# Kernel optimization log

Hardware: AMD Instinct MI355X
Metric: run time of the kernel (lower is better)

## Reference

```python
import jax, jax.numpy as jnp
import numpy as np

EPS = 1e-5
B, H, W = 128, 98, 40

def _conv2d(x, w):
    return jax.lax.conv_general_dilated(x, w, (1, 1), 'VALID', dimension_numbers=('NCHW', 'OIHW', 'NCHW'))

def _bn_ch(x, g, b):
    # BatchNorm over (B,H,W) per channel (training-mode batch stats, as in the torch default mode)
    m = jnp.mean(x, (0, 2, 3), keepdims=True)
    v = jnp.var(x, (0, 2, 3), keepdims=True)
    return (x - m) * jax.lax.rsqrt(v + EPS) * g[None, :, None, None] + b[None, :, None, None]

def _bn_all(x, g, b):
    # BatchNorm3d(1): single channel -> normalize over the whole tensor
    m = jnp.mean(x)
    v = jnp.var(x)
    return (x - m) * jax.lax.rsqrt(v + EPS) * g[0] + b[0]

def _lc(h, w, b):
    # 62 distinct tiny Conv3d(1,1,(3,1,1)) == locally-connected window-3 conv over channel axis: 64 -> 62
    out = b[None, :, None, None]
    for k in range(3):
        out = out + h[:, k:k + 62] * w[None, :, k, None, None]
    return out

def _lc_block(h, lcw, lcb, gs, bs, Wm, bm, gm, bbm):
    h = jax.nn.relu(_bn_all(_lc(h, lcw, lcb), gs, bs))
    # Conv3d kernel (62,1,1): pure channel mixing 62 -> 64 (no relu after, matching torch code)
    h = jnp.einsum('bdhw,cd->bchw', h, Wm) + bm[None, :, None, None]
    return _bn_ch(h, gm, bbm)

def setup_inputs():
    ks = iter(jax.random.split(jax.random.key(0), 64))
    def rn(shape, s=0.05):
        return jax.random.normal(next(ks), shape, jnp.float32) * s
    d = {}
    d['x'] = jax.random.normal(next(ks), (B, H * 0 + 98 if False else 1, 98, 40), jnp.float32) if False else jax.random.normal(next(ks), (B, 1, H, W), jnp.float32)
    d['W11'] = rn((64, 1, 20, 8)); d['b11'] = rn((64,)); d['g11'] = jnp.ones((64,), jnp.float32); d['be11'] = jnp.zeros((64,), jnp.float32)
    d['lc1_w'] = rn((62, 3), 0.3); d['lc1_b'] = rn((62,)); d['g12'] = jnp.ones((1,), jnp.float32); d['be12'] = jnp.zeros((1,), jnp.float32)
    d['W13'] = rn((64, 62)); d['b13'] = rn((64,)); d['g13'] = jnp.ones((64,), jnp.float32); d['be13'] = jnp.zeros((64,), jnp.float32)
    d['W21'] = rn((64, 64, 15, 8), 0.01); d['b21'] = rn((64,)); d['g21'] = jnp.ones((64,), jnp.float32); d['be21'] = jnp.zeros((64,), jnp.float32)
    d['lc2_w'] = rn((62, 3), 0.3); d['lc2_b'] = rn((62,)); d['g22'] = jnp.ones((1,), jnp.float32); d['be22'] = jnp.zeros((1,), jnp.float32)
    d['W23'] = rn((64, 62)); d['b23'] = rn((64,)); d['g23'] = jnp.ones((64,), jnp.float32); d['be23'] = jnp.zeros((64,), jnp.float32)
    d['W31'] = rn((64, 64, 10, 8), 0.01); d['b31'] = rn((64,)); d['g31'] = jnp.ones((64,), jnp.float32); d['be31'] = jnp.zeros((64,), jnp.float32)
    d['lc3_w'] = rn((62, 3), 0.3); d['lc3_b'] = rn((62,)); d['g32'] = jnp.ones((1,), jnp.float32); d['be32'] = jnp.zeros((1,), jnp.float32)
    d['W33'] = rn((64, 62)); d['b33'] = rn((64,)); d['g33'] = jnp.ones((64,), jnp.float32); d['be33'] = jnp.zeros((64,), jnp.float32)
    d['Wf1'] = rn((64, 64 * 56 * 19), 0.01); d['bf1'] = rn((64,)); d['gf'] = jnp.ones((64,), jnp.float32); d['bef'] = jnp.zeros((64,), jnp.float32)
    d['Wf2'] = rn((35, 64)); d['bf2'] = rn((35,))
    return d

def reference(x, W11, b11, g11, be11, lc1_w, lc1_b, g12, be12, W13, b13, g13, be13, W21, b21, g21, be21, lc2_w, lc2_b, g22, be22, W23, b23, g23, be23, W31, b31, g31, be31, lc3_w, lc3_b, g32, be32, W33, b33, g33, be33, Wf1, bf1, gf, bef, Wf2, bf2):
    h = jax.nn.relu(_bn_ch(_conv2d(x, W11) + b11[None, :, None, None], g11, be11))      # [B,64,79,33]
    h = _lc_block(h, lc1_w, lc1_b, g12, be12, W13, b13, g13, be13)                       # [B,64,79,33]
    h = jax.nn.relu(_bn_ch(_conv2d(h, W21) + b21[None, :, None, None], g21, be21))       # [B,64,65,26]
    h = _lc_block(h, lc2_w, lc2_b, g22, be22, W23, b23, g23, be23)                       # [B,64,65,26]
    h = jax.nn.relu(_bn_ch(_conv2d(h, W31) + b31[None, :, None, None], g31, be31))       # [B,64,56,19]
    h = _lc_block(h, lc3_w, lc3_b, g32, be32, W33, b33, g33, be33)                       # [B,64,56,19]
    h = h.reshape(h.shape[0], -1)                                                        # [B,68096]
    h = h @ Wf1.T + bf1
    m = jnp.mean(h, 0)
    v = jnp.var(h, 0)
    h = jax.nn.relu((h - m) * jax.lax.rsqrt(v + EPS) * gf + bef)
    return h @ Wf2.T + bf2
```

## Files before the change

kernel.cpp:

```cpp
#include <hip/hip_runtime.h>

typedef __bf16 bfrag __attribute__((ext_vector_type(8)));
typedef float ffrag __attribute__((ext_vector_type(16)));

constexpr int Bn  = 128;
constexpr int H0  = 98, Wi0 = 40;
constexpr int KH1 = 20, KW1 = 8, H1 = 79, Wo1 = 33, P1 = H1 * Wo1;
constexpr int KH2 = 15, KW2 = 8, H2 = 65, Wo2 = 26, P2 = H2 * Wo2;
constexpr int KH3 = 10, KW3 = 8, H3 = 56, Wo3 = 19, P3 = H3 * Wo3;
constexpr int M1  = Bn * P1;
constexpr int M2  = Bn * P2;
constexpr int M3  = Bn * P3;
constexpr int KFC = 64 * P3;
constexpr int FCCH = 112;
constexpr int FCKL = KFC / FCCH;
constexpr int FCKS = FCKL / 16;
constexpr float EPSF = 1e-5f;

constexpr size_t oA   = 0;
constexpr size_t oB   = oA  + (size_t)Bn * 64 * P1;
constexpr size_t oHB  = oB;
constexpr size_t oWF  = oB  + 4358144;
constexpr size_t oW2  = oB  + (size_t)Bn * 62 * P1;
constexpr size_t oW3  = oW2 + 245760;
constexpr size_t oW1  = oW3 + 163840;
constexpr size_t oWM  = oW1 + 5120;
constexpr size_t oBF  = oWM + 6144;
constexpr size_t oP   = oBF + 128;
constexpr size_t oSt  = oP  + (size_t)FCCH * 8192;
constexpr size_t oF   = oSt + 9 * 512;

__device__ __forceinline__ float wred(float v) {
    #pragma unroll
    for (int o = 32; o > 0; o >>= 1) v += __shfl_down(v, o);
    return v;
}

__device__ __forceinline__ float bank4(const float* stp, int c) {
    return stp[c] + stp[128 + c] + stp[256 + c] + stp[384 + c];
}

constexpr int NZ  = 9 * 512;
constexpr int NW1 = 10240;
constexpr int NWM = 3 * 4096;
constexpr int NPREP = NZ + NW1 + NWM;
__global__ __launch_bounds__(256) void k_prep_all(
    const float* __restrict__ W11, const float* __restrict__ W13,
    const float* __restrict__ W23, const float* __restrict__ W33,
    __bf16* __restrict__ wq1, __bf16* __restrict__ wqm,
    float* __restrict__ st)
{
    int idx = blockIdx.x * 256 + threadIdx.x;
    if (idx < NZ) { st[idx] = 0.f; return; }
    idx -= NZ;
    if (idx < NW1) {
        int j = idx & 7, oc = (idx >> 3) & 63, khh = idx >> 9;
        wq1[idx] = (__bf16)W11[(size_t)oc * 160 + khh * 8 + j];
        return;
    }
    idx -= NW1;
    if (idx < NWM) {
        int which = idx >> 12, r = idx & 4095;
        int j = r & 7, oc = (r >> 3) & 63, sub = (r >> 9) & 1, ks = r >> 10;
        int k = ks * 16 + sub * 8 + j;
        const float* Wm = which == 0 ? W13 : (which == 1 ? W23 : W33);
        wqm[idx] = (k < 62) ? (__bf16)Wm[oc * 62 + k] : (__bf16)0.f;
    }
}

template <int KH, int KW>
__global__ __launch_bounds__(256) void k_foldw(
    const float* __restrict__ W, const float* __restrict__ stp,
    const float* __restrict__ g, const float* __restrict__ be,
    float inv, const float* __restrict__ bias,
    __bf16* __restrict__ wqf, float* __restrict__ biasf)
{
    constexpr int KK = KH * KW;
    __shared__ float sSc[64], sSh[64], ls[4];
    const int t = threadIdx.x;
    if (t < 64) {
        float mm = bank4(stp, t) * inv;
        float vv = bank4(stp, 64 + t) * inv - mm * mm;
        float sc = g[t] * rsqrtf(vv + EPSF);
        sSc[t] = sc;
        sSh[t] = be[t] - mm * sc;
    }
    __syncthreads();
    const int oc = blockIdx.x;
    float local = 0.f;
    for (int i = t; i < 64 * KK; i += 256) {
        int ic = i / KK, rem = i - ic * KK;
        int kh = rem / KW, kw = rem - kh * KW;
        float wv = W[(((size_t)oc * 64 + ic) * KH + kh) * KW + kw];
        int c = ic >> 4, sub = (ic >> 3) & 1, j = ic & 7, pos = kh * KW + kw;
        wqf[(size_t)pos * 4096 + c * 1024 + sub * 512 + oc * 8 + j] = (__bf16)(wv * sSc[ic]);
        local += wv * sSh[ic];
    }
    local = wred(local);
    int wv2 = t >> 6, ln = t & 63;
    if (ln == 0) ls[wv2] = local;
    __syncthreads();
    if (t == 0) biasf[oc] = bias[oc] + ls[0] + ls[1] + ls[2] + ls[3];
}

constexpr int C1COPY = 1736;
__global__ __launch_bounds__(256, 2) void k_conv1m(
    const float* __restrict__ x, const __bf16* __restrict__ wq,
    const float* __restrict__ bias, float* __restrict__ out,
    float* __restrict__ sto)
{
    const int b = blockIdx.y;
    const int m0 = blockIdx.x * 512;
    const int t = threadIdx.x, lane = t & 63, wv = t >> 6;
    const int l31 = lane & 31, lh = lane >> 5;
    __shared__ __align__(16) __bf16 X8[8 * C1COPY];

    const int oh_lo = m0 / Wo1;
    int abase[4];
    #pragma unroll
    for (int mt = 0; mt < 4; ++mt) {
        int m = m0 + wv * 128 + mt * 32 + l31;
        int mc = m > P1 - 1 ? P1 - 1 : m;
        int oh = mc / Wo1, ow = mc - oh * Wo1;
        int s = ow & 7;
        abase[mt] = s * C1COPY + (oh - oh_lo) * 48 + (ow - s);
    }
    for (int idx = t; idx < 8 * 36 * 6; idx += 256) {
        int s = idx / 216; int rr = idx - s * 216;
        int r = rr / 6, q = rr - r * 6;
        int ih = oh_lo + r; if (ih > H0 - 1) ih = H0 - 1;
        const float* src = x + ((size_t)b * H0 + ih) * Wi0;
        __bf16 tmp[8] __attribute__((aligned(16)));
        #pragma unroll
        for (int j = 0; j < 8; ++j) {
            int col = q * 8 + s + j; if (col > Wi0 - 1) col = Wi0 - 1;
            tmp[j] = (__bf16)src[col];
        }
        *(uint4*)&X8[s * C1COPY + r * 48 + q * 8] = *(uint4*)tmp;
    }
    __syncthreads();

    ffrag acc[4][2] = {};
    #pragma unroll 1
    for (int st2 = 0; st2 < 10; ++st2) {
        const int khl = st2 * 2 + lh;
        const __bf16* wp = wq + ((size_t)khl * 64 + l31) * 8;
        bfrag b0 = *(const bfrag*)(wp);
        bfrag b1 = *(const bfrag*)(wp + 256);
        #pragma unroll
        for (int mt = 0; mt < 4; ++mt) {
            bfrag a = *(const bfrag*)&X8[abase[mt] + khl * 48];
            acc[mt][0] = __builtin_amdgcn_mfma_f32_32x32x16_bf16(a, b0, acc[mt][0], 0, 0, 0);
            acc[mt][1] = __builtin_amdgcn_mfma_f32_32x32x16_bf16(a, b1, acc[mt][1], 0, 0, 0);
        }
    }

    float sS[2] = {0.f, 0.f}, sSS[2] = {0.f, 0.f};
    #pragma unroll
    for (int nt = 0; nt < 2; ++nt) {
        int oc = nt * 32 + l31;
        float bv = bias[oc];
        float* op = out + ((size_t)b * 64 + oc) * P1;
        #pragma unroll
        for (int mt = 0; mt < 4; ++mt) {
            int mbase = m0 + wv * 128 + mt * 32 + lh * 4;
            #pragma unroll
            for (int g = 0; g < 4; ++g) {
                int mr = mbase + g * 8;
                float v0 = acc[mt][nt][g * 4 + 0] + bv;
                float v1 = acc[mt][nt][g * 4 + 1] + bv;
                float v2 = acc[mt][nt][g * 4 + 2] + bv;
                float v3 = acc[mt][nt][g * 4 + 3] + bv;
                if (mr + 1 < P1) {
                    *(float2*)(op + mr) = make_float2(v0, v1);
                    sS[nt] += v0 + v1; sSS[nt] += v0 * v0 + v1 * v1;
                    if (mr + 3 < P1) {
                        *(float2*)(op + mr + 2) = make_float2(v2, v3);
                        sS[nt] += v2 + v3; sSS[nt] += v2 * v2 + v3 * v3;
                    } else if (mr + 2 < P1) {
                        op[mr + 2] = v2; sS[nt] += v2; sSS[nt] += v2 * v2;
                    }
                } else if (mr < P1) {
                    op[mr] = v0; sS[nt] += v0; sSS[nt] += v0 * v0;
                }
            }
        }
    }
    #pragma unroll
    for (int nt = 0; nt < 2; ++nt) {
        sS[nt]  += __shfl_down(sS[nt], 32);
        sSS[nt] += __shfl_down(sSS[nt], 32);
    }
    __syncthreads();
    float* redS  = (float*)X8;
    float* redSS = redS + 256;
    if (lane < 32) {
        #pragma unroll
        for (int nt = 0; nt < 2; ++nt) {
            redS[wv * 64 + nt * 32 + l31]  = sS[nt];
            redSS[wv * 64 + nt * 32 + l31] = sSS[nt];
        }
    }
    __syncthreads();
    if (t < 64) {
        int bank = ((blockIdx.x ^ blockIdx.y) & 3) * 128;
        atomicAdd(&sto[bank + t],      redS[t] + redS[64 + t] + redS[128 + t] + redS[192 + t]);
        atomicAdd(&sto[bank + 64 + t], redSS[t] + redSS[64 + t] + redSS[128 + t] + redSS[192 + t]);
    }
}

template <int POS>
__global__ __launch_bounds__(256) void k_lc(const float* __restrict__ in,
                                            const float* __restrict__ stp,
                                            const float* __restrict__ g,
                                            const float* __restrict__ be,
                                            float inv,
                                            const float* __restrict__ lcw,
                                            const float* __restrict__ lcb,
                                            __bf16* __restrict__ Z,
                                            float* __restrict__ sto) {
    __shared__ float sAff[128];
    __shared__ float sred[4], ssred[4];
    if (threadIdx.x < 64) {
        int tt = threadIdx.x;
        float mm = bank4(stp, tt) * inv;
        float vv = bank4(stp, 64 + tt) * inv - mm * mm;
        float sc = g[tt] * rsqrtf(vv + EPSF);
        sAff[tt] = sc;
        sAff[64 + tt] = be[tt] - mm * sc;
    }
    __syncthreads();
    int morig = blockIdx.x * 256 + threadIdx.x;
    bool valid = morig < Bn * POS;
    int m = valid ? morig : Bn * POS - 1;
    int b = m / POS; int p = m - b * POS;
    const float* ip = in + (size_t)b * 64 * POS + p;
    __bf16 zb[64] __attribute__((aligned(16)));
    zb[62] = (__bf16)0.f; zb[63] = (__bf16)0.f;
    float ts = 0.f, tss = 0.f;
    float y0 = fmaxf(sAff[0] * ip[0]           + sAff[64], 0.f);
    float y1 = fmaxf(sAff[1] * ip[(size_t)POS] + sAff[65], 0.f);
    for (int c = 0; c < 62; ++c) {
        float y2 = fmaxf(sAff[c + 2] * ip[(size_t)(c + 2) * POS] + sAff[64 + c + 2], 0.f);
        float o = lcb[c] + y0 * lcw[c * 3] + y1 * lcw[c * 3 + 1] + y2 * lcw[c * 3 + 2];
        zb[c] = (__bf16)o;
        if (valid) { ts += o; tss += o * o; }
        y0 = y1; y1 = y2;
    }
    __bf16* zp = Z + (size_t)m * 64;
    #pragma unroll
    for (int j = 0; j < 8; ++j)
        *(uint4*)(zp + j * 8) = *(uint4*)(zb + j * 8);
    ts = wred(ts); tss = wred(tss);
    int wv = threadIdx.x >> 6, ln = threadIdx.x & 63;
    if (ln == 0) { sred[wv] = ts; ssred[wv] = tss; }
    __syncthreads();
    if (threadIdx.x == 0) {
        int slot = blockIdx.x & 63;
        atomicAdd(&sto[slot],      sred[0] + sred[1] + sred[2] + sred[3]);
        atomicAdd(&sto[64 + slot], ssred[0] + ssred[1] + ssred[2] + ssred[3]);
    }
}

template <int POS, int IH, int IW, bool OUTBF>
__global__ __launch_bounds__(256, 2) void k_mixm(
    const __bf16* __restrict__ Z, const float* __restrict__ stp,
    const float* __restrict__ g, const float* __restrict__ be,
    float inv, const __bf16* __restrict__ wqm,
    const float* __restrict__ bm, void* __restrict__ outv,
    float* __restrict__ sto)
{
    const int b = blockIdx.y;
    const int m0 = blockIdx.x * 512;
    const int t = threadIdx.x, lane = t & 63, wv = t >> 6;
    const int l31 = lane & 31, lh = lane >> 5;

    float gs = 0.f, gss = 0.f;
    #pragma unroll
    for (int i = 0; i < 64; ++i) { gs += stp[i]; gss += stp[64 + i]; }
    float mm = gs * inv;
    float vv = gss * inv - mm * mm;
    float s0 = g[0] * rsqrtf(vv + EPSF);
    float t0 = be[0] - mm * s0;

    size_t zbase[4];
    #pragma unroll
    for (int mt = 0; mt < 4; ++mt) {
        int m = m0 + wv * 128 + mt * 32 + l31;
        int mc = m > POS - 1 ? POS - 1 : m;
        zbase[mt] = ((size_t)b * POS + mc) * 64;
    }

    ffrag acc[4][2] = {};
    #pragma unroll
    for (int ks = 0; ks < 4; ++ks) {
        const __bf16* wp = wqm + ks * 1024 + lh * 512 + l31 * 8;
        bfrag b0 = *(const bfrag*)wp;
        bfrag b1 = *(const bfrag*)(wp + 256);
        #pragma unroll
        for (int mt = 0; mt < 4; ++mt) {
            uint4 raw = *(const uint4*)(Z + zbase[mt] + ks * 16 + lh * 8);
            const __bf16* zin = (const __bf16*)&raw;
            __bf16 zout[8] __attribute__((aligned(16)));
            #pragma unroll
            for (int j = 0; j < 8; ++j) {
                float f = (float)zin[j];
                zout[j] = (__bf16)fmaxf(fmaf(s0, f, t0), 0.f);
            }
            bfrag a = *(const bfrag*)zout;
            acc[mt][0] = __builtin_amdgcn_mfma_f32_32x32x16_bf16(a, b0, acc[mt][0], 0, 0, 0);
            acc[mt][1] = __builtin_amdgcn_mfma_f32_32x32x16_bf16(a, b1, acc[mt][1], 0, 0, 0);
        }
    }

    float sS[2] = {0.f, 0.f}, sSS[2] = {0.f, 0.f};
    #pragma unroll
    for (int nt = 0; nt < 2; ++nt) {
        int oc = nt * 32 + l31;
        float bv = bm[oc];
        if constexpr (OUTBF) {
            __bf16* op = (__bf16*)outv;
            #pragma unroll
            for (int mt = 0; mt < 4; ++mt) {
                int mbase = m0 + wv * 128 + mt * 32 + lh * 4;
                #pragma unroll
                for (int g4 = 0; g4 < 4; ++g4) {
                    #pragma unroll
                    for (int q = 0; q < 4; ++q) {
                        int mr = mbase + g4 * 8 + q;
                        if (mr < POS) {
                            float v = acc[mt][nt][g4 * 4 + q] + bv;
                            int ih = mr / IW, iw = mr - ih * IW;
                            op[((size_t)(b * IH + ih) * 2 + nt) * (IW * 32) + iw * 32 + l31] = (__bf16)v;
                            sS[nt] += v; sSS[nt] += v * v;
                        }
                    }
                }
            }
        } else {
            float* op = (float*)outv + ((size_t)b * 64 + oc) * POS;
            #pragma unroll
            for (int mt = 0; mt < 4; ++mt) {
                int mbase = m0 + wv * 128 + mt * 32 + lh * 4;
                #pragma unroll
                for (int g4 = 0; g4 < 4; ++g4) {
                    int mr = mbase + g4 * 8;
                    if (mr < POS) {
                        float v0 = acc[mt][nt][g4 * 4 + 0] + bv;
                        float v1 = acc[mt][nt][g4 * 4 + 1] + bv;
                        *(float2*)(op + mr) = make_float2(v0, v1);
                        sS[nt] += v0 + v1; sSS[nt] += v0 * v0 + v1 * v1;
                        if (mr + 2 < POS) {
                            float v2 = acc[mt][nt][g4 * 4 + 2] + bv;
                            float v3 = acc[mt][nt][g4 * 4 + 3] + bv;
                            *(float2*)(op + mr + 2) = make_float2(v2, v3);
                            sS[nt] += v2 + v3; sSS[nt] += v2 * v2 + v3 * v3;
                        }
                    }
                }
            }
        }
    }
    #pragma unroll
    for (int nt = 0; nt < 2; ++nt) {
        sS[nt]  += __shfl_down(sS[nt], 32);
        sSS[nt] += __shfl_down(sSS[nt], 32);
    }
    __shared__ float red[512];
    if (lane < 32) {
        #pragma unroll
        for (int nt = 0; nt < 2; ++nt) {
            red[wv * 64 + nt * 32 + l31]       = sS[nt];
            red[256 + wv * 64 + nt * 32 + l31] = sSS[nt];
        }
    }
    __syncthreads();
    if (t < 64) {
        int bank = ((blockIdx.x ^ blockIdx.y) & 3) * 128;
        atomicAdd(&sto[bank + t],      red[t] + red[64 + t] + red[128 + t] + red[192 + t]);
        atomicAdd(&sto[bank + 64 + t], red[256 + t] + red[320 + t] + red[384 + t] + red[448 + t]);
    }
}

template <int KH, int KW, int IH, int IW, int OH, int OW, int NR, int MT>
__global__ __launch_bounds__(256, 2) void k_convmfma(
    const __bf16* __restrict__ in,
    const __bf16* __restrict__ wq,
    const float* __restrict__ bias,
    float* __restrict__ out,
    float* __restrict__ sto)
{
    constexpr int P = OH * OW;
    constexpr int MB = 128 * MT;
    const int b  = blockIdx.y;
    const int m0 = blockIdx.x * MB;
    const int t  = threadIdx.x;
    const int lane = t & 63;
    const int wv = t >> 6;
    const int l31 = lane & 31, lh = lane >> 5;

    __shared__ __align__(16) __bf16 As[NR * IW * 32 + 64];

    const int oh_lo = m0 / OW;
    int posm[MT];
    #pragma unroll
    for (int mt = 0; mt < MT; ++mt) {
        int m = m0 + wv * (32 * MT) + mt * 32 + l31;
        int mc = m > P - 1 ? P - 1 : m;
        int oh = mc / OW, ow = mc - oh * OW;
        posm[mt] = (oh - oh_lo) * IW + ow;
    }

    ffrag acc[MT][2] = {};

    for (int ich = 0; ich < 2; ++ich) {
        __syncthreads();
        constexpr int ROWCH = IW * 4;
        constexpr int CH = NR * ROWCH;
        for (int idx = t; idx < CH; idx += 256) {
            int r = idx / ROWCH, o = idx - r * ROWCH;
            int ih = oh_lo + r; if (ih > IH - 1) ih = IH - 1;
            const __bf16* src = in + ((size_t)(b * IH + ih) * 2 + ich) * (IW * 32) + o * 8;
            int sw = idx ^ ((idx >> 2) & 7);
            *(uint4*)&As[sw * 8] = *(const uint4*)src;
        }
        __syncthreads();

        const __bf16* wich = wq + ich * 2048;
        for (int kh = 0; kh < KH; ++kh) {
            const int rowoff = kh * IW;
            const __bf16* wkh = wich + (size_t)(kh * KW) * 4096 + lh * 512 + l31 * 8;
            #pragma unroll 2
            for (int kw = 0; kw < KW; ++kw) {
                const __bf16* wp = wkh + kw * 4096;
                #pragma unroll
                for (int cc = 0; cc < 2; ++cc) {
                    bfrag b0 = *(const bfrag*)(wp + cc * 1024);
                    bfrag b1 = *(const bfrag*)(wp + cc * 1024 + 256);
                    #pragma unroll
                    for (int mt = 0; mt < MT; ++mt) {
                        int X = posm[mt] + rowoff + kw;
                        int gc = (X << 2) + cc * 2 + lh;
                        bfrag a = *(const bfrag*)&As[(gc ^ (X & 7)) * 8];
                        acc[mt][0] = __builtin_amdgcn_mfma_f32_32x32x16_bf16(a, b0, acc[mt][0], 0, 0, 0);
                        acc[mt][1] = __builtin_amdgcn_mfma_f32_32x32x16_bf16(a, b1, acc[mt][1], 0, 0, 0);
                    }
                }
            }
        }
    }

    float sS[2] = {0.f, 0.f}, sSS[2] = {0.f, 0.f};
    #pragma unroll
    for (int nt = 0; nt < 2; ++nt) {
        int oc = nt * 32 + l31;
        float bv = bias[oc];
        float* op = out + ((size_t)b * 64 + oc) * P;
        #pragma unroll
        for (int mt = 0; mt < MT; ++mt) {
            int mbase = m0 + wv * (32 * MT) + mt * 32 + lh * 4;
            #pragma unroll
            for (int g = 0; g < 4; ++g) {
                int mr = mbase + g * 8;
                if (mr < P) {
                    float v0 = acc[mt][nt][g * 4 + 0] + bv;
                    float v1 = acc[mt][nt][g * 4 + 1] + bv;
                    *(float2*)(op + mr) = make_float2(v0, v1);
                    sS[nt] += v0 + v1; sSS[nt] += v0 * v0 + v1 * v1;
                    if (mr + 2 < P) {
                        float v2 = acc[mt][nt][g * 4 + 2] + bv;
                        float v3 = acc[mt][nt][g * 4 + 3] + bv;
                        *(float2*)(op + mr + 2) = make_float2(v2, v3);
                        sS[nt] += v2 + v3; sSS[nt] += v2 * v2 + v3 * v3;
                    }
                }
            }
        }
    }
    #pragma unroll
    for (int nt = 0; nt < 2; ++nt) {
        sS[nt]  += __shfl_down(sS[nt], 32);
        sSS[nt] += __shfl_down(sSS[nt], 32);
    }
    __syncthreads();
    float* redS  = (float*)As;
    float* redSS = redS + 256;
    if (lane < 32) {
        #pragma unroll
        for (int nt = 0; nt < 2; ++nt) {
            redS[wv * 64 + nt * 32 + l31]  = sS[nt];
            redSS[wv * 64 + nt * 32 + l31] = sSS[nt];
        }
    }
    __syncthreads();
    if (t < 64) {
        int bank = ((blockIdx.x ^ blockIdx.y) & 3) * 128;
        atomicAdd(&sto[bank + t],      redS[t] + redS[64 + t] + redS[128 + t] + redS[192 + t]);
        atomicAdd(&sto[bank + 64 + t], redSS[t] + redSS[64 + t] + redSS[128 + t] + redSS[192 + t]);
    }
}

constexpr int NHB  = M3 * 64 / 8;
constexpr int NWFB = 64 * KFC / 8;
__global__ __launch_bounds__(256) void k_prep_hb(
    const float* __restrict__ Y, const float* __restrict__ stp,
    const float* __restrict__ g, const float* __restrict__ be, float inv,
    const float* __restrict__ Wf1,
    __bf16* __restrict__ hb, __bf16* __restrict__ wf1b)
{
    int idx = blockIdx.x * 256 + threadIdx.x;
    if (idx < NHB) {
        size_t base = (size_t)idx * 8;
        int c = (int)(base / P3) & 63;
        float mm = bank4(stp, c) * inv;
        float vv = bank4(stp, 64 + c) * inv - mm * mm;
        float sc = g[c] * rsqrtf(vv + EPSF);
        float sh = be[c] - mm * sc;
        __bf16 tmp[8] __attribute__((aligned(16)));
        #pragma unroll
        for (int j = 0; j < 8; ++j)
            tmp[j] = (__bf16)(sc * Y[base + j] + sh);
        *(uint4*)(hb + base) = *(uint4*)tmp;
        return;
    }
    idx -= NHB;
    if (idx < NWFB) {
        size_t base = (size_t)idx * 8;
        __bf16 tmp[8] __attribute__((aligned(16)));
        #pragma unroll
        for (int j = 0; j < 8; ++j)
            tmp[j] = (__bf16)Wf1[base + j];
        *(uint4*)(wf1b + base) = *(uint4*)tmp;
    }
}

__global__ __launch_bounds__(256) void k_fc1m(const __bf16* __restrict__ hb,
                                              const __bf16* __restrict__ wf1b,
                                              float* __restrict__ Pb) {
    const int kc = blockIdx.x;
    const int t = threadIdx.x, lane = t & 63, wv = t >> 6;
    const int l31 = lane & 31, lh = lane >> 5;
    const int k0 = kc * FCKL;

    const __bf16* ap = hb + (size_t)(wv * 32 + l31) * KFC + k0 + lh * 8;
    const __bf16* bp0 = wf1b + (size_t)l31 * KFC + k0 + lh * 8;
    const __bf16* bp1 = wf1b + (size_t)(32 + l31) * KFC + k0 + lh * 8;

    ffrag acc[2] = {};
    #pragma unroll 2
    for (int ks = 0; ks < FCKS; ++ks) {
        bfrag a  = *(const bfrag*)(ap  + ks * 16);
        bfrag b0 = *(const bfrag*)(bp0 + ks * 16);
        bfrag b1 = *(const bfrag*)(bp1 + ks * 16);
        acc[0] = __builtin_amdgcn_mfma_f32_32x32x16_bf16(a, b0, acc[0], 0, 0, 0);
        acc[1] = __builtin_amdgcn_mfma_f32_32x32x16_bf16(a, b1, acc[1], 0, 0, 0);
    }
    float* pp = Pb + (size_t)kc * 8192;
    #pragma unroll
    for (int nt = 0; nt < 2; ++nt) {
        #pragma unroll
        for (int g = 0; g < 4; ++g) {
            #pragma unroll
            for (int q = 0; q < 4; ++q) {
                int row = q + g * 8 + lh * 4;
                int bb = wv * 32 + row;
                pp[bb * 64 + nt * 32 + l31] = acc[nt][g * 4 + q];
            }
        }
    }
}

__global__ __launch_bounds__(256) void k_fc1red(const float* __restrict__ Pb,
                                                float* __restrict__ F) {
    int m = blockIdx.x * 256 + threadIdx.x;
    float s = 0.f;
    for (int kc = 0; kc < FCCH; ++kc) s += Pb[(size_t)kc * 8192 + m];
    F[m] = s;
}

__global__ __launch_bounds__(256) void k_fcfin(const float* __restrict__ F,
                                               const float* __restrict__ bf1,
                                               const float* __restrict__ gf,
                                               const float* __restrict__ bef,
                                               const float* __restrict__ Wf2,
                                               const float* __restrict__ bf2,
                                               float* __restrict__ out) {
    __shared__ float sF[8192];
    __shared__ float sfa[128];
    const int t = threadIdx.x;
    for (int m = t; m < 8192; m += 256) sF[m] = F[m];
    __syncthreads();
    if (t < 64) {
        float s = 0.f, ss = 0.f;
        for (int b = 0; b < Bn; ++b) {
            float v = sF[b * 64 + t] + bf1[t];
            s += v; ss += v * v;
        }
        float m  = s / 128.f;
        float va = ss / 128.f - m * m;
        float sc = gf[t] * rsqrtf(va + EPSF);
        sfa[t] = sc;
        sfa[64 + t] = sc * bf1[t] + bef[t] - m * sc;
    }
    __syncthreads();
    for (int m = t; m < Bn * 35; m += 256) {
        int b = m / 35, o = m - b * 35;
        float acc = bf2[o];
        for (int ff = 0; ff < 64; ++ff) {
            int f = (ff + t) & 63;
            float z = fmaxf(sfa[f] * sF[b * 64 + f] + sfa[64 + f], 0.f);
            acc += z * Wf2[o * 64 + f];
        }
        out[m] = acc;
    }
}

extern "C" void kernel_launch(void* const* d_in, const int* in_sizes, int n_in,
                              void* d_out, int out_size, void* d_ws, size_t ws_size,
                              hipStream_t stream) {
    const float* x    = (const float*)d_in[0];
    const float* W11  = (const float*)d_in[1];
    const float* b11  = (const float*)d_in[2];
    const float* g11  = (const float*)d_in[3];
    const float* be11 = (const float*)d_in[4];
    const float* lc1w = (const float*)d_in[5];
    const float* lc1b = (const float*)d_in[6];
    const float* g12  = (const float*)d_in[7];
    const float* be12 = (const float*)d_in[8];
    const float* W13  = (const float*)d_in[9];
    const float* b13  = (const float*)d_in[10];
    const float* g13  = (const float*)d_in[11];
    const float* be13 = (const float*)d_in[12];
    const float* W21  = (const float*)d_in[13];
    const float* b21  = (const float*)d_in[14];
    const float* g21  = (const float*)d_in[15];
    const float* be21 = (const float*)d_in[16];
    const float* lc2w = (const float*)d_in[17];
    const float* lc2b = (const float*)d_in[18];
    const float* g22  = (const float*)d_in[19];
    const float* be22 = (const float*)d_in[20];
    const float* W23  = (const float*)d_in[21];
    const float* b23  = (const float*)d_in[22];
    const float* g23  = (const float*)d_in[23];
    const float* be23 = (const float*)d_in[24];
    const float* W31  = (const float*)d_in[25];
    const float* b31  = (const float*)d_in[26];
    const float* g31  = (const float*)d_in[27];
    const float* be31 = (const float*)d_in[28];
    const float* lc3w = (const float*)d_in[29];
    const float* lc3b = (const float*)d_in[30];
    const float* g32  = (const float*)d_in[31];
    const float* be32 = (const float*)d_in[32];
    const float* W33  = (const float*)d_in[33];
    const float* b33  = (const float*)d_in[34];
    const float* g33  = (const float*)d_in[35];
    const float* be33 = (const float*)d_in[36];
    const float* Wf1  = (const float*)d_in[37];
    const float* bf1  = (const float*)d_in[38];
    const float* gf   = (const float*)d_in[39];
    const float* bef  = (const float*)d_in[40];
    const float* Wf2  = (const float*)d_in[41];
    const float* bf2  = (const float*)d_in[42];

    float* ws  = (float*)d_ws;
    float* A   = ws + oA;
    float* Bb  = ws + oB;
    __bf16* Abf = (__bf16*)(ws + oA);
    __bf16* Bbf = (__bf16*)(ws + oB);
    __bf16* hb   = (__bf16*)(ws + oHB);
    __bf16* wf1b = (__bf16*)(ws + oWF);
    __bf16* wq2f = (__bf16*)(ws + oW2);
    __bf16* wq3f = (__bf16*)(ws + oW3);
    __bf16* wq1  = (__bf16*)(ws + oW1);
    __bf16* wqm  = (__bf16*)(ws + oWM);
    float* bfold = ws + oBF;
    float* Pb  = ws + oP;
    float* st  = ws + oSt;
    float* F   = ws + oF;

    const int blk1 = (M1 + 255) / 256;
    const int blk2 = M2 / 256;
    const int blk3 = M3 / 256;

    k_prep_all<<<(NPREP + 255) / 256, 256, 0, stream>>>(W11, W13, W23, W33, wq1, wqm, st);

    k_conv1m<<<dim3((P1 + 511) / 512, Bn), 256, 0, stream>>>(x, wq1, b11, A, st + 0 * 512);
    k_lc<P1><<<blk1, 256, 0, stream>>>(A, st + 0 * 512, g11, be11, 1.0f / (float)M1,
                                       lc1w, lc1b, Bbf, st + 1 * 512);
    k_mixm<P1, H1, Wo1, true><<<dim3((P1 + 511) / 512, Bn), 256, 0, stream>>>(
        Bbf, st + 1 * 512, g12, be12, 1.0f / (62.0f * (float)M1),
        wqm + 0 * 4096, b13, (void*)Abf, st + 2 * 512);

    k_foldw<KH2, KW2><<<64, 256, 0, stream>>>(W21, st + 2 * 512, g13, be13,
                                              1.0f / (float)M1, b21, wq2f, bfold + 0);
    k_convmfma<KH2, KW2, H1, Wo1, H2, Wo2, 35, 4>
        <<<dim3((P2 + 511) / 512, Bn), 256, 0, stream>>>(Abf, wq2f, bfold + 0, Bb, st + 3 * 512);
    k_lc<P2><<<blk2, 256, 0, stream>>>(Bb, st + 3 * 512, g21, be21, 1.0f / (float)M2,
                                       lc2w, lc2b, Abf, st + 4 * 512);
    k_mixm<P2, H2, Wo2, true><<<dim3((P2 + 511) / 512, Bn), 256, 0, stream>>>(
        Abf, st + 4 * 512, g22, be22, 1.0f / (62.0f * (float)M2),
        wqm + 1 * 4096, b23, (void*)Bbf, st + 5 * 512);

    k_foldw<KH3, KW3><<<64, 256, 0, stream>>>(W31, st + 5 * 512, g23, be23,
                                              1.0f / (float)M2, b31, wq3f, bfold + 64);
    k_convmfma<KH3, KW3, H2, Wo2, H3, Wo3, 30, 3>
        <<<dim3((P3 + 383) / 384, Bn), 256, 0, stream>>>(Bbf, wq3f, bfold + 64, A, st + 6 * 512);
    k_lc<P3><<<blk3, 256, 0, stream>>>(A, st + 6 * 512, g31, be31, 1.0f / (float)M3,
                                       lc3w, lc3b, Bbf, st + 7 * 512);
    k_mixm<P3, 1, 1, false><<<dim3((P3 + 511) / 512, Bn), 256, 0, stream>>>(
        Bbf, st + 7 * 512, g32, be32, 1.0f / (62.0f * (float)M3),
        wqm + 2 * 4096, b33, (void*)A, st + 8 * 512);

    k_prep_hb<<<(NHB + NWFB + 255) / 256, 256, 0, stream>>>(
        A, st + 8 * 512, g33, be33, 1.0f / (float)M3, Wf1, hb, wf1b);
    k_fc1m<<<FCCH, 256, 0, stream>>>(hb, wf1b, Pb);
    k_fc1red<<<32, 256, 0, stream>>>(Pb, F);
    k_fcfin<<<1, 256, 0, stream>>>(F, bf1, gf, bef, Wf2, bf2, (float*)d_out);
}
```

Baseline: 909.6 us.

## Switch fp32 intermediate activations to channel-last layout and re-swizzle LDS

Conv epilogues now write fp32 outputs position-major with channels innermost (NHWC) instead of channel-planar. The locally-connected kernel can then read each position's 64 channels as contiguous float4 loads rather than 64 strided loads. The FC prep kernel is adapted: BN affine params are computed once per block into shared memory, and Wf1 is permuted during bf16 conversion to match the new flattening order. The LDS swizzle in the conv tile loader also gains an extra XOR term to cut bank conflicts. The trade-off is that epilogue stores become scalar writes with a 256-byte stride, and the Wf1 conversion now gathers with a stride of P3.

```diff
diff --git a/kernel.cpp b/kernel.cpp
--- a/kernel.cpp
+++ b/kernel.cpp
@@ -160,28 +160,20 @@
     for (int nt = 0; nt < 2; ++nt) {
         int oc = nt * 32 + l31;
         float bv = bias[oc];
-        float* op = out + ((size_t)b * 64 + oc) * P1;
+        float* op = out + (size_t)b * P1 * 64 + oc;
         #pragma unroll
         for (int mt = 0; mt < 4; ++mt) {
             int mbase = m0 + wv * 128 + mt * 32 + lh * 4;
             #pragma unroll
             for (int g = 0; g < 4; ++g) {
-                int mr = mbase + g * 8;
-                float v0 = acc[mt][nt][g * 4 + 0] + bv;
-                float v1 = acc[mt][nt][g * 4 + 1] + bv;
-                float v2 = acc[mt][nt][g * 4 + 2] + bv;
-                float v3 = acc[mt][nt][g * 4 + 3] + bv;
-                if (mr + 1 < P1) {
-                    *(float2*)(op + mr) = make_float2(v0, v1);
-                    sS[nt] += v0 + v1; sSS[nt] += v0 * v0 + v1 * v1;
-                    if (mr + 3 < P1) {
-                        *(float2*)(op + mr + 2) = make_float2(v2, v3);
-                        sS[nt] += v2 + v3; sSS[nt] += v2 * v2 + v3 * v3;
-                    } else if (mr + 2 < P1) {
-                        op[mr + 2] = v2; sS[nt] += v2; sSS[nt] += v2 * v2;
+                #pragma unroll
+                for (int q = 0; q < 4; ++q) {
+                    int mr = mbase + g * 8 + q;
+                    if (mr < P1) {
+                        float v = acc[mt][nt][g * 4 + q] + bv;
+                        op[(size_t)mr * 64] = v;
+                        sS[nt] += v; sSS[nt] += v * v;
                     }
-                } else if (mr < P1) {
-                    op[mr] = v0; sS[nt] += v0; sSS[nt] += v0 * v0;
                 }
             }
         }
@@ -233,15 +225,19 @@
     int morig = blockIdx.x * 256 + threadIdx.x;
     bool valid = morig < Bn * POS;
     int m = valid ? morig : Bn * POS - 1;
-    int b = m / POS; int p = m - b * POS;
-    const float* ip = in + (size_t)b * 64 * POS + p;
+    const float* ip = in + (size_t)m * 64;
+    float xv[64];
+    #pragma unroll
+    for (int j = 0; j < 16; ++j)
+        *(float4*)&xv[j * 4] = *(const float4*)(ip + j * 4);
     __bf16 zb[64] __attribute__((aligned(16)));
     zb[62] = (__bf16)0.f; zb[63] = (__bf16)0.f;
     float ts = 0.f, tss = 0.f;
-    float y0 = fmaxf(sAff[0] * ip[0]           + sAff[64], 0.f);
-    float y1 = fmaxf(sAff[1] * ip[(size_t)POS] + sAff[65], 0.f);
+    float y0 = fmaxf(sAff[0] * xv[0] + sAff[64], 0.f);
+    float y1 = fmaxf(sAff[1] * xv[1] + sAff[65], 0.f);
+    #pragma unroll
     for (int c = 0; c < 62; ++c) {
-        float y2 = fmaxf(sAff[c + 2] * ip[(size_t)(c + 2) * POS] + sAff[64 + c + 2], 0.f);
+        float y2 = fmaxf(sAff[c + 2] * xv[c + 2] + sAff[64 + c + 2], 0.f);
         float o = lcb[c] + y0 * lcw[c * 3] + y1 * lcw[c * 3 + 1] + y2 * lcw[c * 3 + 2];
         zb[c] = (__bf16)o;
         if (valid) { ts += o; tss += o * o; }
@@ -338,23 +334,19 @@
                 }
             }
         } else {
-            float* op = (float*)outv + ((size_t)b * 64 + oc) * POS;
+            float* op = (float*)outv + (size_t)b * POS * 64 + oc;
             #pragma unroll
             for (int mt = 0; mt < 4; ++mt) {
                 int mbase = m0 + wv * 128 + mt * 32 + lh * 4;
                 #pragma unroll
                 for (int g4 = 0; g4 < 4; ++g4) {
-                    int mr = mbase + g4 * 8;
-                    if (mr < POS) {
-                        float v0 = acc[mt][nt][g4 * 4 + 0] + bv;
-                        float v1 = acc[mt][nt][g4 * 4 + 1] + bv;
-                        *(float2*)(op + mr) = make_float2(v0, v1);
-                        sS[nt] += v0 + v1; sSS[nt] += v0 * v0 + v1 * v1;
-                        if (mr + 2 < POS) {
-                            float v2 = acc[mt][nt][g4 * 4 + 2] + bv;
-                            float v3 = acc[mt][nt][g4 * 4 + 3] + bv;
-                            *(float2*)(op + mr + 2) = make_float2(v2, v3);
-                            sS[nt] += v2 + v3; sSS[nt] += v2 * v2 + v3 * v3;
+                    #pragma unroll
+                    for (int q = 0; q < 4; ++q) {
+                        int mr = mbase + g4 * 8 + q;
+                        if (mr < POS) {
+                            float v = acc[mt][nt][g4 * 4 + q] + bv;
+                            op[(size_t)mr * 64] = v;
+                            sS[nt] += v; sSS[nt] += v * v;
                         }
                     }
                 }
@@ -421,7 +413,8 @@
             int r = idx / ROWCH, o = idx - r * ROWCH;
             int ih = oh_lo + r; if (ih > IH - 1) ih = IH - 1;
             const __bf16* src = in + ((size_t)(b * IH + ih) * 2 + ich) * (IW * 32) + o * 8;
-            int sw = idx ^ ((idx >> 2) & 7);
+            int Xw = idx >> 2;
+            int sw = idx ^ ((Xw ^ (Xw >> 3)) & 7);
             *(uint4*)&As[sw * 8] = *(const uint4*)src;
         }
         __syncthreads();
@@ -441,7 +434,8 @@
                     for (int mt = 0; mt < MT; ++mt) {
                         int X = posm[mt] + rowoff + kw;
                         int gc = (X << 2) + cc * 2 + lh;
-                        bfrag a = *(const bfrag*)&As[(gc ^ (X & 7)) * 8];
+                        int sw = gc ^ ((X ^ (X >> 3)) & 7);
+                        bfrag a = *(const bfrag*)&As[sw * 8];
                         acc[mt][0] = __builtin_amdgcn_mfma_f32_32x32x16_bf16(a, b0, acc[mt][0], 0, 0, 0);
                         acc[mt][1] = __builtin_amdgcn_mfma_f32_32x32x16_bf16(a, b1, acc[mt][1], 0, 0, 0);
                     }
@@ -455,23 +449,19 @@
     for (int nt = 0; nt < 2; ++nt) {
         int oc = nt * 32 + l31;
         float bv = bias[oc];
-        float* op = out + ((size_t)b * 64 + oc) * P;
+        float* op = out + (size_t)b * P * 64 + oc;
         #pragma unroll
         for (int mt = 0; mt < MT; ++mt) {
             int mbase = m0 + wv * (32 * MT) + mt * 32 + lh * 4;
             #pragma unroll
             for (int g = 0; g < 4; ++g) {
-                int mr = mbase + g * 8;
-                if (mr < P) {
-                    float v0 = acc[mt][nt][g * 4 + 0] + bv;
-                    float v1 = acc[mt][nt][g * 4 + 1] + bv;
-                    *(float2*)(op + mr) = make_float2(v0, v1);
-                    sS[nt] += v0 + v1; sSS[nt] += v0 * v0 + v1 * v1;
-                    if (mr + 2 < P) {
-                        float v2 = acc[mt][nt][g * 4 + 2] + bv;
-                        float v3 = acc[mt][nt][g * 4 + 3] + bv;
-                        *(float2*)(op + mr + 2) = make_float2(v2, v3);
-                        sS[nt] += v2 + v3; sSS[nt] += v2 * v2 + v3 * v3;
+                #pragma unroll
+                for (int q = 0; q < 4; ++q) {
+                    int mr = mbase + g * 8 + q;
+                    if (mr < P) {
+                        float v = acc[mt][nt][g * 4 + q] + bv;
+                        op[(size_t)mr * 64] = v;
+                        sS[nt] += v; sSS[nt] += v * v;
                     }
                 }
             }
@@ -508,28 +498,36 @@
     const float* __restrict__ Wf1,
     __bf16* __restrict__ hb, __bf16* __restrict__ wf1b)
 {
+    __shared__ float sA[128];
+    if (threadIdx.x < 64) {
+        int c = threadIdx.x;
+        float mm = bank4(stp, c) * inv;
+        float vv = bank4(stp, 64 + c) * inv - mm * mm;
+        float sc = g[c] * rsqrtf(vv + EPSF);
+        sA[c] = sc; sA[64 + c] = be[c] - mm * sc;
+    }
+    __syncthreads();
     int idx = blockIdx.x * 256 + threadIdx.x;
     if (idx < NHB) {
         size_t base = (size_t)idx * 8;
-        int c = (int)(base / P3) & 63;
-        float mm = bank4(stp, c) * inv;
-        float vv = bank4(stp, 64 + c) * inv - mm * mm;
-        float sc = g[c] * rsqrtf(vv + EPSF);
-        float sh = be[c] - mm * sc;
+        int c0 = (int)(base & 63);
         __bf16 tmp[8] __attribute__((aligned(16)));
         #pragma unroll
         for (int j = 0; j < 8; ++j)
-            tmp[j] = (__bf16)(sc * Y[base + j] + sh);
+            tmp[j] = (__bf16)(sA[c0 + j] * Y[base + j] + sA[64 + c0 + j]);
         *(uint4*)(hb + base) = *(uint4*)tmp;
         return;
     }
     idx -= NHB;
     if (idx < NWFB) {
         size_t base = (size_t)idx * 8;
+        int f = (int)(base / KFC);
+        int r = (int)(base - (size_t)f * KFC);
+        int p = r >> 6, c0 = r & 63;
         __bf16 tmp[8] __attribute__((aligned(16)));
         #pragma unroll
         for (int j = 0; j < 8; ++j)
-            tmp[j] = (__bf16)Wf1[base + j];
+            tmp[j] = (__bf16)Wf1[(size_t)f * KFC + (size_t)(c0 + j) * P3 + p];
         *(uint4*)(wf1b + base) = *(uint4*)tmp;
     }
 }
```

Measured after the change: 897.8 us. No clear change (-1.3%).
